# Performance work log

Hardware: AMD Instinct MI355X
Metric: run time of the kernel (lower is better)

Reference implementation:

```python
import jax, jax.numpy as jnp
import numpy as np

PC_RANGE = (-50.0, -50.0, -4.0, 50.0, 50.0, 4.0)
IMG_H, IMG_W = 256.0, 704.0
EPS = 1e-5


def _bilinear_sample(feat, u, v):
    # feat [H,W,C]; u,v [M] in [0,1]; matches F.grid_sample(align_corners=False, padding_mode='zeros')
    H, W, _ = feat.shape
    x = u * W - 0.5
    y = v * H - 0.5
    x0 = jnp.floor(x)
    y0 = jnp.floor(y)
    dx = (x - x0)[:, None]
    dy = (y - y0)[:, None]
    x0 = x0.astype(jnp.int32)
    y0 = y0.astype(jnp.int32)

    def g(xi, yi):
        inb = ((xi >= 0) & (xi < W) & (yi >= 0) & (yi < H)).astype(feat.dtype)[:, None]
        return feat[jnp.clip(yi, 0, H - 1), jnp.clip(xi, 0, W - 1)] * inb

    return (g(x0, y0) * (1 - dx) * (1 - dy) + g(x0 + 1, y0) * dx * (1 - dy)
            + g(x0, y0 + 1) * (1 - dx) * dy + g(x0 + 1, y0 + 1) * dx * dy)


def _conv1x1(t, w, b):
    return jnp.einsum('bchw,oc->bohw', t, w) + b[None, :, None, None]


def _inorm(t, eps=1e-5):
    # InstanceNorm2d (affine=False): normalize per (b, c) over spatial dims
    m = t.mean(axis=(2, 3), keepdims=True)
    var = t.var(axis=(2, 3), keepdims=True)
    return (t - m) * jax.lax.rsqrt(var + eps)


def _forward(feat, lidar2img, bev_pos, pe_w1, pe_b1, pe_w2, pe_b2, pe_w3, pe_b3,
             c1_w, c1_b, c2_w, c2_b, c3_w, c3_b):
    B, N, C, Hf, Wf = feat.shape
    _, P, Hb, Wb, _ = bev_pos.shape
    Q = Hb * Wb
    lo = jnp.asarray(PC_RANGE[:3], feat.dtype)
    hi = jnp.asarray(PC_RANGE[3:], feat.dtype)
    # 'b p h w d -> b (h w) p d', then scale normalized coords into pc_range
    ref01 = jnp.transpose(bev_pos, (0, 2, 3, 1, 4)).reshape(B, Q, P, 3)
    ref = ref01 * (hi - lo) + lo
    # project through per-camera lidar2img (homogeneous)
    pts = jnp.concatenate([ref, jnp.ones_like(ref[..., :1])], axis=-1)  # [B,Q,P,4]
    cam = jnp.einsum('bnij,bqpj->bnqpi', lidar2img, pts)                # [B,N,Q,P,4]
    homo = cam[..., 2]
    z = jnp.maximum(homo, EPS)
    u = cam[..., 0] / z / IMG_W
    v = cam[..., 1] / z / IMG_H
    valid = ((homo > EPS) & (u > 0.0) & (u < 1.0) & (v > 0.0) & (v < 1.0)).astype(feat.dtype)
    # bilinear gather per camera; feats to channel-last ('b n (g c) h w -> (b g) n h w c', G=1)
    fmap = jnp.transpose(feat, (0, 1, 3, 4, 2)).reshape(B * N, Hf, Wf, C)
    samp = jax.vmap(_bilinear_sample)(fmap, u.reshape(B * N, Q * P), v.reshape(B * N, Q * P))
    samp = samp.reshape(B, N, Q, P, C) * valid[..., None]
    samp = samp.sum(axis=1)  # sum over cameras -> [B,Q,P,C]
    # PositionalEncodingMap(3 -> 256 -> 256 -> 128) on normalized reference points
    pe = jax.nn.relu(ref01 @ pe_w1 + pe_b1)
    pe = jax.nn.relu(pe @ pe_w2 + pe_b2)
    pe = pe @ pe_w3 + pe_b3
    samp = samp + pe
    # 'b (h w) g p c -> b (p g c) h w' with g=1
    x = jnp.transpose(samp.reshape(B, Hb, Wb, P, C), (0, 3, 4, 1, 2)).reshape(B, P * C, Hb, Wb)
    gelu = lambda t: jax.nn.gelu(t, approximate=False)
    x = gelu(_inorm(_conv1x1(x, c1_w, c1_b)))
    x = gelu(_inorm(_conv1x1(x, c2_w, c2_b)))
    x = _conv1x1(x, c3_w, c3_b)
    return x


def setup_inputs() -> dict:
    key = jax.random.key(0)
    ks = jax.random.split(key, 16)
    B, N, C, Hf, Wf = 1, 6, 128, 32, 88
    P, Hb, Wb = 4, 160, 160
    E = 128
    MID = 256
    s = 0.02
    return {
        'feat': jax.random.normal(ks[0], (B, N, C, Hf, Wf), jnp.float32),
        'lidar2img': jax.random.normal(ks[1], (B, N, 4, 4), jnp.float32),
        'bev_pos': jax.random.uniform(ks[2], (B, P, Hb, Wb, 3), jnp.float32),
        'pe_w1': jax.random.normal(ks[3], (3, MID), jnp.float32) * s,
        'pe_b1': jnp.zeros((MID,), jnp.float32),
        'pe_w2': jax.random.normal(ks[4], (MID, MID), jnp.float32) * s,
        'pe_b2': jnp.zeros((MID,), jnp.float32),
        'pe_w3': jax.random.normal(ks[5], (MID, E), jnp.float32) * s,
        'pe_b3': jnp.zeros((E,), jnp.float32),
        'c1_w': jax.random.normal(ks[6], (4 * E, P * 128), jnp.float32) * s,
        'c1_b': jnp.zeros((4 * E,), jnp.float32),
        'c2_w': jax.random.normal(ks[7], (E, 4 * E), jnp.float32) * s,
        'c2_b': jnp.zeros((E,), jnp.float32),
        'c3_w': jax.random.normal(ks[8], (E, E), jnp.float32) * s,
        'c3_b': jnp.zeros((E,), jnp.float32),
    }


def reference(feat, lidar2img, bev_pos, pe_w1, pe_b1, pe_w2, pe_b2, pe_w3, pe_b3,
              c1_w, c1_b, c2_w, c2_b, c3_w, c3_b):
    return _forward(feat, lidar2img, bev_pos, pe_w1, pe_b1, pe_w2, pe_b2, pe_w3, pe_b3,
                    c1_w, c1_b, c2_w, c2_b, c3_w, c3_b)
```

## Files before the change

### kernel.cpp

```cpp
#include <hip/hip_runtime.h>
#include <cstdint>
#include <cstddef>

using frag8 = __attribute__((ext_vector_type(8))) short;
using f32x4 = __attribute__((ext_vector_type(4))) float;

__device__ __forceinline__ float b2f_bits(unsigned short u) {
    union { uint32_t u32; float f; } x; x.u32 = ((uint32_t)u) << 16; return x.f;
}
__device__ __forceinline__ float b2f_lo(uint32_t pk) {
    return __builtin_bit_cast(float, pk << 16);
}
__device__ __forceinline__ float b2f_hi(uint32_t pk) {
    return __builtin_bit_cast(float, pk & 0xffff0000u);
}
__device__ __forceinline__ unsigned short f2b(float f) {
    uint32_t u = __builtin_bit_cast(uint32_t, f);
    uint32_t r = (u + 0x7fffu + ((u >> 16) & 1u)) >> 16;
    return (unsigned short)r;
}
__device__ __forceinline__ uint32_t cvtpk_bf16(float lo, float hi) {
    uint32_t r;
    asm("v_cvt_pk_bf16_f32 %0, %1, %2" : "=v"(r) : "v"(lo), "v"(hi));
    return r;
}

#define HF 32
#define WFEAT 88
#define NCAM 6
#define NPT 102400
#define BM 128
#define BN 128
#define BK 64

__global__ __launch_bounds__(256) void k_prep(const float* __restrict__ feat,
                                              const float* __restrict__ pw2,
                                              const float* __restrict__ pw3,
                                              const float* __restrict__ c1w,
                                              const float* __restrict__ c2w,
                                              const float* __restrict__ c3w,
                                              const float* __restrict__ l2i,
                                              const float* __restrict__ bev,
                                              unsigned short* __restrict__ featT,
                                              unsigned short* __restrict__ W2Tb,
                                              unsigned short* __restrict__ W3Tb,
                                              unsigned short* __restrict__ C1Wb,
                                              unsigned short* __restrict__ C2Wb,
                                              unsigned short* __restrict__ C3Wb,
                                              float* __restrict__ stats,
                                              int* __restrict__ poff,
                                              float4* __restrict__ pwts) {
    __shared__ unsigned short tile[64 * 132];
    int b = blockIdx.x, t = threadIdx.x;
    if (b < 2400) {
        int idx = b * 256 + t;
        int n = idx / NPT, pt = idx - n * NPT;
        int q = pt >> 2, p = pt & 3;
        int h = q / 160, w = q - h * 160;
        const float* bv = bev + ((p * 160 + h) * 160 + w) * 3;
        float rx = bv[0] * 100.f - 50.f;
        float ry = bv[1] * 100.f - 50.f;
        float rz = bv[2] * 8.f - 4.f;
        const float* M = l2i + n * 16;
        float c0   = M[0] * rx + M[1] * ry + M[2]  * rz + M[3];
        float c1v  = M[4] * rx + M[5] * ry + M[6]  * rz + M[7];
        float homo = M[8] * rx + M[9] * ry + M[10] * rz + M[11];
        float z = fmaxf(homo, 1e-5f);
        float u = c0 / z / 704.0f;
        float v = c1v / z / 256.0f;
        if (!(homo > 1e-5f && u > 0.f && u < 1.f && v > 0.f && v < 1.f)) {
            poff[idx] = -1;
            return;
        }
        float fx = u * (float)WFEAT - 0.5f;
        float fy = v * (float)HF - 0.5f;
        float fx0 = floorf(fx), fy0 = floorf(fy);
        float dx = fx - fx0, dy = fy - fy0;
        int x0 = (int)fx0, y0 = (int)fy0;
        float wxa = (x0 < 0) ? dx : 1.f - dx;
        float wxb = (x0 >= 0 && x0 < WFEAT - 1) ? dx : 0.f;
        float wya = (y0 < 0) ? dy : 1.f - dy;
        float wyb = (y0 >= 0 && y0 < HF - 1) ? dy : 0.f;
        int bx = max(x0, 0), by = max(y0, 0);
        poff[idx] = ((n * HF + by) * WFEAT + bx) << 7;
        pwts[idx] = make_float4(wxa * wya, wxb * wya, wxa * wyb, wxb * wyb);
        return;
    }
    b -= 2400;
    if (b < 264) {
        int n = b / 44;
        int s0 = (b - n * 44) * 64;
        #pragma unroll
        for (int i = 0; i < 32; ++i) {
            int e = i * 256 + t;
            int c = e >> 6, sl = e & 63;
            tile[sl * 132 + c] = f2b(feat[(size_t)(n * 128 + c) * 2816 + s0 + sl]);
        }
        __syncthreads();
        #pragma unroll
        for (int j = 0; j < 8; ++j) {
            int flat = j * 1024 + t * 4;
            int sl = flat >> 7, c = flat & 127;
            ushort4 v = *(const ushort4*)(tile + sl * 132 + c);
            *(ushort4*)(featT + (size_t)(n * 2816 + s0 + sl) * 128 + c) = v;
        }
        return;
    }
    b -= 264;
    if (b < 256) {
        int idx = b * 256 + t;
        int r = idx >> 8, c = idx & 255;
        W2Tb[c * 256 + r] = f2b(pw2[idx]);
        return;
    }
    b -= 256;
    if (b < 128) {
        int idx = b * 256 + t;
        int r = idx >> 7, c = idx & 127;
        W3Tb[c * 256 + r] = f2b(pw3[idx]);
        return;
    }
    b -= 128;
    if (b < 1024) { int idx = b * 256 + t; C1Wb[idx] = f2b(c1w[idx]); return; }
    b -= 1024;
    if (b < 256)  { int idx = b * 256 + t; C2Wb[idx] = f2b(c2w[idx]); return; }
    b -= 256;
    if (b < 64)   { int idx = b * 256 + t; C3Wb[idx] = f2b(c3w[idx]); return; }
    #pragma unroll
    for (int j = 0; j < 10; ++j) stats[t * 10 + j] = 0.f;
}

__global__ __launch_bounds__(256) void k_sample2(const unsigned short* __restrict__ featT,
                                                 const int* __restrict__ poff,
                                                 const float4* __restrict__ pwts,
                                                 unsigned short* __restrict__ samp) {
    int pt = blockIdx.x * 4 + (threadIdx.x >> 6);
    int lane = threadIdx.x & 63;
    int c2 = lane * 2;
    int offs[NCAM];
    float4 ww[NCAM];
    #pragma unroll
    for (int n = 0; n < NCAM; ++n) offs[n] = poff[n * NPT + pt];
    #pragma unroll
    for (int n = 0; n < NCAM; ++n) ww[n] = pwts[n * NPT + pt];
    float acc0 = 0.f, acc1 = 0.f;
    #pragma unroll
    for (int n = 0; n < NCAM; ++n) {
        if (offs[n] >= 0) {
            const unsigned short* base = featT + offs[n] + c2;
            uint32_t p00 = *(const uint32_t*)(base);
            uint32_t p01 = *(const uint32_t*)(base + 128);
            uint32_t p10 = *(const uint32_t*)(base + WFEAT * 128);
            uint32_t p11 = *(const uint32_t*)(base + WFEAT * 128 + 128);
            float4 w = ww[n];
            acc0 += w.x * b2f_lo(p00) + w.y * b2f_lo(p01) + w.z * b2f_lo(p10) + w.w * b2f_lo(p11);
            acc1 += w.x * b2f_hi(p00) + w.y * b2f_hi(p01) + w.z * b2f_hi(p10) + w.w * b2f_hi(p11);
        }
    }
    uint32_t outpk = (uint32_t)f2b(acc0) | ((uint32_t)f2b(acc1) << 16);
    *(uint32_t*)(samp + (size_t)pt * 128 + c2) = outpk;
}

__device__ __forceinline__ void stage_tile(const unsigned short* __restrict__ g, int ld,
                                           unsigned short* lds, int wave, int lane) {
    #pragma unroll
    for (int j = 0; j < 4; ++j) {
        int idx = wave * 256 + j * 64 + lane;
        int r = idx >> 3;
        int cs = idx & 7;
        int cl = cs ^ (r & 7);
        __builtin_amdgcn_global_load_lds(
            (const __attribute__((address_space(1))) void*)(g + (size_t)r * ld + cl * 8),
            (__attribute__((address_space(3))) void*)(lds + wave * 2048 + j * 512),
            16, 0, 0);
    }
}

__device__ __forceinline__ frag8 frag_read(const unsigned short* lds, int row, int chunk) {
    return *(const frag8*)(lds + row * 64 + ((chunk ^ (row & 7)) << 3));
}

__device__ __forceinline__ void mma_tile(const unsigned short* As, const unsigned short* Bs,
                                         int wm, int wn, int lane, f32x4 (&acc)[4][4]) {
    int lm = lane & 15, lq = lane >> 4;
    #pragma unroll
    for (int kk = 0; kk < 2; ++kk) {
        frag8 a[4], b[4];
        #pragma unroll
        for (int t = 0; t < 4; ++t) a[t] = frag_read(As, wm * 64 + t * 16 + lm, kk * 4 + lq);
        #pragma unroll
        for (int t = 0; t < 4; ++t) b[t] = frag_read(Bs, wn * 64 + t * 16 + lm, kk * 4 + lq);
        #pragma unroll
        for (int tm = 0; tm < 4; ++tm)
            #pragma unroll
            for (int tn = 0; tn < 4; ++tn)
                acc[tm][tn] = __builtin_amdgcn_mfma_f32_16x16x32_bf16(a[tm], b[tn], acc[tm][tn], 0, 0, 0);
    }
}

template <int KT>
__device__ __forceinline__ void gemm_loop_pipe(const unsigned short* __restrict__ A, int ldA,
                                               const unsigned short* __restrict__ B, int ldB,
                                               unsigned short (*As)[BM * BK],
                                               unsigned short (*Bs)[BN * BK],
                                               int wave, int lane, int wm, int wn,
                                               f32x4 (&acc)[4][4]) {
    stage_tile(A, ldA, As[0], wave, lane);
    stage_tile(B, ldB, Bs[0], wave, lane);
    if (KT > 1) {
        stage_tile(A + BK, ldA, As[1], wave, lane);
        stage_tile(B + BK, ldB, Bs[1], wave, lane);
    }
    #pragma unroll
    for (int kt = 0; kt < KT; ++kt) {
        int cur = kt & 1;
        if (kt + 1 < KT) asm volatile("s_waitcnt vmcnt(8)" ::: "memory");
        else             asm volatile("s_waitcnt vmcnt(0)" ::: "memory");
        __builtin_amdgcn_s_barrier();
        mma_tile(As[cur], Bs[cur], wm, wn, lane, acc);
        asm volatile("s_waitcnt lgkmcnt(0)" ::: "memory");
        __builtin_amdgcn_s_barrier();
        if (kt + 2 < KT) {
            stage_tile(A + (kt + 2) * BK, ldA, As[cur], wave, lane);
            stage_tile(B + (kt + 2) * BK, ldB, Bs[cur], wave, lane);
        }
    }
}

__device__ __forceinline__ void build_h1(const float* __restrict__ wls, float x, float y, float z,
                                         int r, int c0, int kt, unsigned short* __restrict__ As) {
    #pragma unroll
    for (int j = 0; j < 4; ++j) {
        int cl = c0 + j;
        const float* wp = wls + kt * 64 + cl * 8;
        float4 a0l = *(const float4*)(wp),       a0h = *(const float4*)(wp + 4);
        float4 a1l = *(const float4*)(wp + 256), a1h = *(const float4*)(wp + 260);
        float4 a2l = *(const float4*)(wp + 512), a2h = *(const float4*)(wp + 516);
        float4 bbl = *(const float4*)(wp + 768), bbh = *(const float4*)(wp + 772);
        float v0 = fmaxf(x * a0l.x + y * a1l.x + z * a2l.x + bbl.x, 0.f);
        float v1 = fmaxf(x * a0l.y + y * a1l.y + z * a2l.y + bbl.y, 0.f);
        float v2 = fmaxf(x * a0l.z + y * a1l.z + z * a2l.z + bbl.z, 0.f);
        float v3 = fmaxf(x * a0l.w + y * a1l.w + z * a2l.w + bbl.w, 0.f);
        float v4 = fmaxf(x * a0h.x + y * a1h.x + z * a2h.x + bbh.x, 0.f);
        float v5 = fmaxf(x * a0h.y + y * a1h.y + z * a2h.y + bbh.y, 0.f);
        float v6 = fmaxf(x * a0h.z + y * a1h.z + z * a2h.z + bbh.z, 0.f);
        float v7 = fmaxf(x * a0h.w + y * a1h.w + z * a2h.w + bbh.w, 0.f);
        uint32_t q0 = cvtpk_bf16(v0, v1), q1 = cvtpk_bf16(v2, v3);
        uint32_t q2 = cvtpk_bf16(v4, v5), q3 = cvtpk_bf16(v6, v7);
        *(uint4*)(As + r * 64 + ((cl ^ (r & 7)) << 3)) = make_uint4(q0, q1, q2, q3);
    }
}

__global__ __launch_bounds__(256) void k_pe12(const float* __restrict__ bev,
                                              const float* __restrict__ pw1,
                                              const float* __restrict__ pb1,
                                              const unsigned short* __restrict__ Bt,
                                              const float* __restrict__ bias,
                                              unsigned short* __restrict__ H2) {
    __shared__ unsigned short As[BM * BK], Bs[BN * BK];
    __shared__ __align__(16) float wls[4 * 256];
    __shared__ float bevs[3 * 128];
    int t = threadIdx.x, lane = t & 63, wave = t >> 6;
    int wm = wave >> 1, wn = wave & 1;
    int m0 = blockIdx.x * BM, n0 = blockIdx.y * BN;
    {
        int i = t * 4;
        int j = i >> 8, c = i & 255;
        float4 v = (j < 3) ? *(const float4*)(pw1 + j * 256 + c)
                           : *(const float4*)(pb1 + c);
        *(float4*)(wls + i) = v;
    }
    if (t < 128) {
        int m = m0 + t;
        int q = m >> 2, p = m & 3;
        int h = q / 160, w = q - h * 160;
        const float* bv = bev + ((size_t)((p * 160 + h) * 160 + w)) * 3;
        bevs[t] = bv[0]; bevs[128 + t] = bv[1]; bevs[256 + t] = bv[2];
    }
    __syncthreads();
    int r = t & 127;
    int c0 = (t >> 7) * 4;
    float x = bevs[r], y = bevs[128 + r], z = bevs[256 + r];
    f32x4 acc[4][4] = {};
    for (int kt = 0; kt < 4; ++kt) {
        stage_tile(Bt + (size_t)n0 * 256 + kt * BK, 256, Bs, wave, lane);
        build_h1(wls, x, y, z, r, c0, kt, As);
        __syncthreads();
        mma_tile(As, Bs, wm, wn, lane, acc);
        __syncthreads();
    }
    int lm = lane & 15, lq = lane >> 4;
    #pragma unroll
    for (int tn = 0; tn < 4; ++tn) {
        int n = n0 + wn * 64 + tn * 16 + lm;
        float bn = bias[n];
        #pragma unroll
        for (int tm = 0; tm < 4; ++tm) {
            int mb = m0 + wm * 64 + tm * 16 + lq * 4;
            #pragma unroll
            for (int rr = 0; rr < 4; ++rr)
                H2[(size_t)(mb + rr) * 256 + n] = f2b(fmaxf(acc[tm][tn][rr] + bn, 0.f));
        }
    }
}

__global__ __launch_bounds__(256) void k_gemm_pe3(const unsigned short* __restrict__ A,
                                                  const unsigned short* __restrict__ Bt,
                                                  const float* __restrict__ bias,
                                                  const unsigned short* __restrict__ samp,
                                                  unsigned short* __restrict__ X) {
    __shared__ unsigned short As[2][BM * BK], Bs[2][BN * BK];
    int lane = threadIdx.x & 63, wave = threadIdx.x >> 6;
    int wm = wave >> 1, wn = wave & 1;
    int m0 = blockIdx.x * BM;
    f32x4 acc[4][4] = {};
    gemm_loop_pipe<4>(A + (size_t)m0 * 256, 256, Bt, 256, As, Bs, wave, lane, wm, wn, acc);
    int lm = lane & 15, lq = lane >> 4;
    #pragma unroll
    for (int tn = 0; tn < 4; ++tn) {
        int n = wn * 64 + tn * 16 + lm;
        float bn = bias[n];
        #pragma unroll
        for (int tm = 0; tm < 4; ++tm) {
            int mb = m0 + wm * 64 + tm * 16 + lq * 4;
            #pragma unroll
            for (int rr = 0; rr < 4; ++rr) {
                size_t off = (size_t)(mb + rr) * 128 + n;
                X[off] = f2b(acc[tm][tn][rr] + bn + b2f_bits(samp[off]));
            }
        }
    }
}

template <int K, bool STATS>
__global__ __launch_bounds__(256) void k_gemm_conv(const unsigned short* __restrict__ A,
                                                   const unsigned short* __restrict__ Bt,
                                                   const float* __restrict__ bias,
                                                   unsigned short* __restrict__ Y, int ldY,
                                                   float* __restrict__ st, int C) {
    __shared__ unsigned short As[2][BM * BK], Bs[2][BN * BK];
    int lane = threadIdx.x & 63, wave = threadIdx.x >> 6;
    int wm = wave >> 1, wn = wave & 1;
    int m0 = blockIdx.x * BM, n0 = blockIdx.y * BN;
    f32x4 acc[4][4] = {};
    gemm_loop_pipe<K / BK>(A + (size_t)m0 * K, K, Bt + (size_t)n0 * K, K,
                           As, Bs, wave, lane, wm, wn, acc);
    int lm = lane & 15, lq = lane >> 4;
    #pragma unroll
    for (int tn = 0; tn < 4; ++tn) {
        int n = n0 + wn * 64 + tn * 16 + lm;
        float bn = bias[n];
        float s1 = 0.f, s2 = 0.f;
        #pragma unroll
        for (int tm = 0; tm < 4; ++tm) {
            int mb = m0 + wm * 64 + tm * 16 + lq * 4;
            #pragma unroll
            for (int rr = 0; rr < 4; ++rr) {
                float v = acc[tm][tn][rr] + bn;
                Y[(size_t)(mb + rr) * ldY + n] = f2b(v);
                if (STATS) { s1 += v; s2 += v * v; }
            }
        }
        if (STATS) {
            s1 += __shfl_xor(s1, 16); s1 += __shfl_xor(s1, 32);
            s2 += __shfl_xor(s2, 16); s2 += __shfl_xor(s2, 32);
            if (lq == 0) { atomicAdd(&st[n], s1); atomicAdd(&st[C + n], s2); }
        }
    }
}

__global__ __launch_bounds__(256) void k_gemm_conv3(const unsigned short* __restrict__ A,
                                                    const unsigned short* __restrict__ Bt,
                                                    const float* __restrict__ bias,
                                                    float* __restrict__ out) {
    __shared__ unsigned short As[2][BM * BK], Bs[2][BN * BK];
    int lane = threadIdx.x & 63, wave = threadIdx.x >> 6;
    int wm = wave >> 1, wn = wave & 1;
    int m0 = blockIdx.x * BM;
    f32x4 acc[4][4] = {};
    gemm_loop_pipe<2>(A + (size_t)m0 * 128, 128, Bt, 128, As, Bs, wave, lane, wm, wn, acc);
    int lm = lane & 15, lq = lane >> 4;
    #pragma unroll
    for (int tn = 0; tn < 4; ++tn) {
        int n = wn * 64 + tn * 16 + lm;
        float bn = bias[n];
        #pragma unroll
        for (int tm = 0; tm < 4; ++tm) {
            int mb = m0 + wm * 64 + tm * 16 + lq * 4;
            float4 pk;
            pk.x = acc[tm][tn][0] + bn;
            pk.y = acc[tm][tn][1] + bn;
            pk.z = acc[tm][tn][2] + bn;
            pk.w = acc[tm][tn][3] + bn;
            *(float4*)(out + (size_t)n * 25600 + mb) = pk;
        }
    }
}

__global__ void k_normgelu8f(const unsigned short* __restrict__ Y, const float* __restrict__ st,
                             unsigned short* __restrict__ X2, int Cmask, int C, float inv_n,
                             int total8) {
    int i8 = blockIdx.x * 256 + threadIdx.x;
    if (i8 >= total8) return;
    int e0 = i8 * 8;
    int c = e0 & Cmask;
    uint4 y = *(const uint4*)(Y + e0);
    float4 s1a = *(const float4*)(st + c);
    float4 s1b = *(const float4*)(st + c + 4);
    float4 s2a = *(const float4*)(st + C + c);
    float4 s2b = *(const float4*)(st + C + c + 4);
    float mu[8] = { s1a.x * inv_n, s1a.y * inv_n, s1a.z * inv_n, s1a.w * inv_n,
                    s1b.x * inv_n, s1b.y * inv_n, s1b.z * inv_n, s1b.w * inv_n };
    float sq[8] = { s2a.x, s2a.y, s2a.z, s2a.w, s2b.x, s2b.y, s2b.z, s2b.w };
    float rs[8];
    #pragma unroll
    for (int j = 0; j < 8; ++j) rs[j] = rsqrtf(sq[j] * inv_n - mu[j] * mu[j] + 1e-5f);
    const float is2 = 0.70710678118654752f;
    unsigned int yw[4] = {y.x, y.y, y.z, y.w};
    unsigned int ow[4];
    #pragma unroll
    for (int j = 0; j < 4; ++j) {
        float v0 = (b2f_bits((unsigned short)(yw[j] & 0xffffu)) - mu[j * 2]) * rs[j * 2];
        float v1 = (b2f_bits((unsigned short)(yw[j] >> 16)) - mu[j * 2 + 1]) * rs[j * 2 + 1];
        float g0 = 0.5f * v0 * (1.f + erff(v0 * is2));
        float g1 = 0.5f * v1 * (1.f + erff(v1 * is2));
        ow[j] = (uint32_t)f2b(g0) | ((uint32_t)f2b(g1) << 16);
    }
    *(uint4*)(X2 + e0) = make_uint4(ow[0], ow[1], ow[2], ow[3]);
}

extern "C" void kernel_launch(void* const* d_in, const int* in_sizes, int n_in,
                              void* d_out, int out_size, void* d_ws, size_t ws_size,
                              hipStream_t stream) {
    (void)in_sizes; (void)n_in; (void)out_size; (void)ws_size;
    const float* feat = (const float*)d_in[0];
    const float* l2i  = (const float*)d_in[1];
    const float* bev  = (const float*)d_in[2];
    const float* pw1  = (const float*)d_in[3];
    const float* pb1  = (const float*)d_in[4];
    const float* pw2  = (const float*)d_in[5];
    const float* pb2  = (const float*)d_in[6];
    const float* pw3  = (const float*)d_in[7];
    const float* pb3  = (const float*)d_in[8];
    const float* c1w  = (const float*)d_in[9];
    const float* c1b  = (const float*)d_in[10];
    const float* c2w  = (const float*)d_in[11];
    const float* c2b  = (const float*)d_in[12];
    const float* c3w  = (const float*)d_in[13];
    const float* c3b  = (const float*)d_in[14];
    float* outp = (float*)d_out;
    char* ws = (char*)d_ws;

    unsigned short* featT = (unsigned short*)(ws + 0);
    unsigned short* W2Tb  = (unsigned short*)(ws + 4348416);
    unsigned short* W3Tb  = (unsigned short*)(ws + 4479488);
    unsigned short* C1Wb  = (unsigned short*)(ws + 4545024);
    unsigned short* C2Wb  = (unsigned short*)(ws + 5069312);
    unsigned short* C3Wb  = (unsigned short*)(ws + 5200384);
    float* stats          = (float*)(ws + 5233152);
    int*    poff          = (int*)(ws + 5247488);
    float4* pwts          = (float4*)(ws + 7705088);
    char* BUF1 = ws + 17535488;
    char* BUF2 = ws + 69964288;
    char* BUF3 = ws + 122393088;

    float* st512 = stats;
    float* st128 = stats + 2048;

    unsigned short* H2   = (unsigned short*)BUF2;
    unsigned short* samp = (unsigned short*)BUF3;
    unsigned short* X    = (unsigned short*)BUF1;
    unsigned short* Y1   = (unsigned short*)BUF2;
    unsigned short* X2   = (unsigned short*)BUF3;
    unsigned short* Y2   = (unsigned short*)BUF1;
    unsigned short* X3   = (unsigned short*)(BUF1 + 6553600);

    k_prep<<<4393, 256, 0, stream>>>(feat, pw2, pw3, c1w, c2w, c3w, l2i, bev,
                                     featT, W2Tb, W3Tb, C1Wb, C2Wb, C3Wb, stats,
                                     poff, pwts);

    k_sample2<<<25600, 256, 0, stream>>>(featT, poff, pwts, samp);

    k_pe12<<<dim3(800, 2), 256, 0, stream>>>(bev, pw1, pb1, W2Tb, pb2, H2);
    k_gemm_pe3<<<dim3(800, 1), 256, 0, stream>>>(H2, W3Tb, pb3, samp, X);

    k_gemm_conv<512, true><<<dim3(200, 4), 256, 0, stream>>>(X, C1Wb, c1b, Y1, 512, st512, 512);
    k_normgelu8f<<<6400, 256, 0, stream>>>(Y1, st512, X2, 511, 512, 1.f / 25600.f, 1638400);

    k_gemm_conv<512, true><<<dim3(200, 1), 256, 0, stream>>>(X2, C2Wb, c2b, Y2, 128, st128, 128);
    k_normgelu8f<<<1600, 256, 0, stream>>>(Y2, st128, X3, 127, 128, 1.f / 25600.f, 409600);

    k_gemm_conv3<<<200, 256, 0, stream>>>(X3, C3Wb, c3b, outp);
}
```

Before: 269.9 us.

## Compute full N=256 per block in pe12 to avoid rebuilding H1 twice

The fused PE layer-1/layer-2 kernel now covers all 256 output columns in one block instead of splitting N across two grid columns. Before, each of the two blocks recomputed the same layer-1 activations (build_h1) and reloaded bev. Each wave now holds a 4x8 accumulator tile and stages both halves of the weight tile, which halves the grid and the redundant layer-1 work. The cost is more accumulator registers and a larger LDS footprint, which may lower occupancy.

```diff
diff --git a/kernel.cpp b/kernel.cpp
--- a/kernel.cpp
+++ b/kernel.cpp
@@ -257,12 +257,13 @@
                                               const unsigned short* __restrict__ Bt,
                                               const float* __restrict__ bias,
                                               unsigned short* __restrict__ H2) {
-    __shared__ unsigned short As[BM * BK], Bs[BN * BK];
+    __shared__ unsigned short As[BM * BK];
+    __shared__ unsigned short Bs[256 * BK];
     __shared__ __align__(16) float wls[4 * 256];
     __shared__ float bevs[3 * 128];
     int t = threadIdx.x, lane = t & 63, wave = t >> 6;
     int wm = wave >> 1, wn = wave & 1;
-    int m0 = blockIdx.x * BM, n0 = blockIdx.y * BN;
+    int m0 = blockIdx.x * BM;
     {
         int i = t * 4;
         int j = i >> 8, c = i & 255;
@@ -281,18 +282,35 @@
     int r = t & 127;
     int c0 = (t >> 7) * 4;
     float x = bevs[r], y = bevs[128 + r], z = bevs[256 + r];
-    f32x4 acc[4][4] = {};
+    int lm = lane & 15, lq = lane >> 4;
+    f32x4 acc[4][8] = {};
     for (int kt = 0; kt < 4; ++kt) {
-        stage_tile(Bt + (size_t)n0 * 256 + kt * BK, 256, Bs, wave, lane);
+        stage_tile(Bt + kt * BK, 256, Bs, wave, lane);
+        stage_tile(Bt + 128 * 256 + kt * BK, 256, Bs + 8192, wave, lane);
         build_h1(wls, x, y, z, r, c0, kt, As);
         __syncthreads();
-        mma_tile(As, Bs, wm, wn, lane, acc);
+        #pragma unroll
+        for (int kk = 0; kk < 2; ++kk) {
+            int ch = kk * 4 + lq;
+            frag8 a[4], b[8];
+            #pragma unroll
+            for (int tt = 0; tt < 4; ++tt) a[tt] = frag_read(As, wm * 64 + tt * 16 + lm, ch);
+            #pragma unroll
+            for (int tn = 0; tn < 8; ++tn) {
+                int brow = (tn < 4 ? wn * 64 + tn * 16 : 128 + wn * 64 + (tn - 4) * 16) + lm;
+                b[tn] = frag_read(Bs, brow, ch);
+            }
+            #pragma unroll
+            for (int tm = 0; tm < 4; ++tm)
+                #pragma unroll
+                for (int tn = 0; tn < 8; ++tn)
+                    acc[tm][tn] = __builtin_amdgcn_mfma_f32_16x16x32_bf16(a[tm], b[tn], acc[tm][tn], 0, 0, 0);
+        }
         __syncthreads();
     }
-    int lm = lane & 15, lq = lane >> 4;
-    #pragma unroll
-    for (int tn = 0; tn < 4; ++tn) {
-        int n = n0 + wn * 64 + tn * 16 + lm;
+    #pragma unroll
+    for (int tn = 0; tn < 8; ++tn) {
+        int n = (tn < 4 ? wn * 64 + tn * 16 : 128 + wn * 64 + (tn - 4) * 16) + lm;
         float bn = bias[n];
         #pragma unroll
         for (int tm = 0; tm < 4; ++tm) {
@@ -481,7 +499,7 @@
 
     k_sample2<<<25600, 256, 0, stream>>>(featT, poff, pwts, samp);
 
-    k_pe12<<<dim3(800, 2), 256, 0, stream>>>(bev, pw1, pb1, W2Tb, pb2, H2);
+    k_pe12<<<800, 256, 0, stream>>>(bev, pw1, pb1, W2Tb, pb2, H2);
     k_gemm_pe3<<<dim3(800, 1), 256, 0, stream>>>(H2, W3Tb, pb3, samp, X);
 
     k_gemm_conv<512, true><<<dim3(200, 4), 256, 0, stream>>>(X, C1Wb, c1b, Y1, 512, st512, 512);
```

Measured after the change: 278.5 us. +3.2%, slower.
